# Kernel optimization log

Hardware: AMD Instinct MI355X
Metric: run time of the kernel (lower is better)

The kernel has to match this reference:

```python
import jax, jax.numpy as jnp
import numpy as np

B, T, S, L, R, H, UE = 64, 256, 16, 128, 16, 256, 64


def setup_inputs() -> dict:
    key = jax.random.key(0)
    ks = jax.random.split(key, 10)
    u = jax.random.normal(ks[0], (B, T, UE), jnp.float32)
    k = 0.1 * jax.random.normal(ks[1], (B, T, L), jnp.float32)
    K = 0.1 * jax.random.normal(ks[2], (B, T, L, R), jnp.float32)
    eps_z = jax.random.normal(ks[3], (T, S, B, L), jnp.float32)
    eps_w = jax.random.normal(ks[4], (T, S, B, R), jnp.float32)
    W1 = jax.random.normal(ks[5], (L, H), jnp.float32) / np.sqrt(L).astype(np.float32)
    W2 = jax.random.normal(ks[6], (H, L), jnp.float32) / np.sqrt(H).astype(np.float32)
    m_init = jax.random.normal(ks[7], (L,), jnp.float32)
    Q_diag = jax.random.uniform(ks[8], (L,), jnp.float32, 0.1, 1.0)
    Q0_diag = jax.random.uniform(ks[9], (L,), jnp.float32, 0.5, 1.5)
    return dict(u=u, k=k, K=K, eps_z=eps_z, eps_w=eps_w, W1=W1, W2=W2,
                m_init=m_init, Q_diag=Q_diag, Q0_diag=Q0_diag, n_samples=S)


def reference(u, k, K, eps_z, eps_w, W1, W2, m_init, Q_diag, Q0_diag, n_samples):
    Bn, Tn, Ln, Rn = K.shape
    ue = u.shape[-1]
    I_r = jnp.eye(Rn, dtype=K.dtype)

    def bmv(A, x):      # A: [B,L,R], x: [...,B,R] -> [...,B,L]
        return jnp.einsum('blr,...br->...bl', A, x)

    def bmvT(A, x):     # A: [B,L,R], x: [...,B,L] -> [...,B,R]
        return jnp.einsum('blr,...bl->...br', A, x)

    def mean_fn(z):
        return z + jnp.tanh(z @ W1) @ W2

    def step_core(m, K_t, k_t, ez, ew, q_a):
        # A = I + K^T diag(q_a) K  (rank x rank)
        A = I_r + jnp.einsum('blr,l,blq->brq', K_t, q_a, K_t)
        Lc = jnp.linalg.cholesky(A)
        Linv = jax.scipy.linalg.solve_triangular(
            Lc, jnp.broadcast_to(I_r, Lc.shape), lower=True)

        def csolve(x):  # solve A y = x via Linv^T Linv x
            y = jnp.einsum('bij,...bj->...bi', Linv, x)
            return jnp.einsum('bji,...bj->...bi', Linv, y)

        # gain direction; inner shift always uses Q_diag (as in torch source)
        g = k_t - bmv(K_t, csolve(bmvT(K_t, m + Q_diag * k_t)))
        m_f = m + q_a * g
        z_p = jnp.sqrt(q_a) * ez
        z_f = m_f + z_p - bmv(K_t, csolve(bmvT(K_t, z_p) + ew))
        qp = jnp.sum(q_a * g * g, axis=-1)
        M = A - I_r  # = K^T diag(q_a) K
        tr = -jnp.einsum('bij,bjk,bik->b', Linv, M, Linv)
        logdet = 2.0 * jnp.sum(jnp.log(jnp.diagonal(Lc, axis1=-2, axis2=-1)), axis=-1)
        kl = 0.5 * (qp + tr + logdet)
        return z_f, m_f, z_p, kl

    # ---- t = 0 (uses initial covariance Q0_diag) ----
    m0 = jnp.broadcast_to(m_init, (Bn, Ln))
    m0 = m0.at[:, :ue].add(u[:, 0])
    z_f0, m_f0, z_p0, kl0 = step_core(m0, K[:, 0], k[:, 0], eps_z[0], eps_w[0], Q0_diag)

    # ---- t = 1..T-1: sequential nonlinear filter scan ----
    def scan_fn(z_prev, xs):
        u_t, k_t, K_t, ez, ew = xs
        m = mean_fn(z_prev)            # [S,B,L]
        m = m.at[..., :ue].add(u_t)    # broadcast input over samples
        z_f, m_f, z_p, kl = step_core(m, K_t, k_t, ez, ew, Q_diag)
        return z_f, (z_f, m_f.mean(axis=0), z_p, kl.mean(axis=0))

    xs = (jnp.swapaxes(u[:, 1:], 0, 1),
          jnp.swapaxes(k[:, 1:], 0, 1),
          jnp.swapaxes(K[:, 1:], 0, 1),
          eps_z[1:], eps_w[1:])
    _, (z_fs, m_fs, z_ps, kls) = jax.lax.scan(scan_fn, z_f0, xs)

    z_f = jnp.transpose(jnp.concatenate([z_f0[None], z_fs], 0), (1, 2, 0, 3))  # [S,B,T,L]
    m_f = jnp.transpose(jnp.concatenate([m_f0[None], m_fs], 0), (1, 0, 2))     # [B,T,L]
    z_p = jnp.transpose(jnp.concatenate([z_p0[None], z_ps], 0), (1, 2, 0, 3))  # [S,B,T,L]
    kl = jnp.concatenate([kl0[None], kls], 0).T                                 # [B,T]
    return z_f, m_f, z_p, kl
```

## Files before the change

kernel.cpp:

```cpp
#include <hip/hip_runtime.h>
#include <cstddef>

typedef _Float16 half8v __attribute__((ext_vector_type(8)));
typedef _Float16 half4v __attribute__((ext_vector_type(4)));
typedef float f32x4 __attribute__((ext_vector_type(4)));

#define MFMA32(A, B, C) __builtin_amdgcn_mfma_f32_16x16x32_f16(A, B, C, 0, 0, 0)
#define MFMA16(A, B, C) __builtin_amdgcn_mfma_f32_16x16x16f16(A, B, C, 0, 0, 0)

__global__ void kw2_kernel(const float* __restrict__ W2, _Float16* __restrict__ w2h) {
  int i = blockIdx.x * 256 + threadIdx.x;
  w2h[i] = (_Float16)W2[i];
}

#define BAR() asm volatile("s_waitcnt lgkmcnt(0)\n\ts_barrier" ::: "memory")

template <bool PK, bool ZW>
__device__ __forceinline__ void scan_body(
    const int b, const int ct,
    _Float16* __restrict__ svhc, _Float16* __restrict__ hbc,
    float (*__restrict__ h2pc)[320], float (*__restrict__ qppc)[64],
    const float* __restrict__ ug, const float* __restrict__ Kg,
    const float* __restrict__ W1, const float* __restrict__ W2,
    const float* __restrict__ m_init, const float* __restrict__ Qd,
    const float* __restrict__ Q0d, const _Float16* __restrict__ pfb,
    const float* __restrict__ cgp, const _Float16* __restrict__ rfb,
    const _Float16* __restrict__ kab, const float* __restrict__ zpcb,
    const float* __restrict__ klcp, float* __restrict__ out_zf,
    float* __restrict__ out_mf, float* __restrict__ out_kl) {
  const int wvc = ct >> 6;
  const int ln = ct & 63;
  const int g = ln >> 4;
  const int c = ln & 15;

  half8v w1f[4][4];
#pragma unroll
  for (int mt = 0; mt < 4; ++mt)
#pragma unroll
    for (int kt = 0; kt < 4; ++kt) {
      half8v v;
#pragma unroll
      for (int j = 0; j < 8; ++j)
        v[j] = (_Float16)W1[(size_t)(kt * 32 + g * 8 + j) * 256 + (wvc * 64 + mt * 16 + c)];
      w1f[mt][kt] = v;
    }
  half8v w2f[2][8];
#pragma unroll
  for (int mt = 0; mt < 2; ++mt)
#pragma unroll
    for (int kt = 0; kt < 8; ++kt) {
      half8v v;
#pragma unroll
      for (int j = 0; j < 8; ++j)
        v[j] = (_Float16)W2[(size_t)(kt * 32 + g * 8 + j) * 128 + (wvc * 32 + mt * 16 + c)];
      w2f[mt][kt] = v;
    }

  f32x4 qiv[2], qiv0[2];
#pragma unroll
  for (int mt = 0; mt < 2; ++mt) {
    f32x4 q = *(const f32x4*)&Qd[wvc * 32 + mt * 16 + g * 4];
    f32x4 q0 = *(const f32x4*)&Q0d[wvc * 32 + mt * 16 + g * 4];
#pragma unroll
    for (int r = 0; r < 4; ++r) { qiv[mt][r] = 1.f / q[r]; qiv0[mt][r] = 1.f / q0[r]; }
  }

  f32x4 zreg[2];

  half8v pfx0, pfx1, kax0 = {}, kax1 = {}, rfa0, rfa1, rfc0, rfc1;
  float kf0[8], kf1[8];
  f32x4 zq0[2], zq1[2], cv0[2], cv1[2];
  f32x4 ur0[2] = {}, ur1[2] = {};
  float kv0 = 0.f, kv1 = 0.f;

  const char* pf_p = (const char*)pfb + (size_t)b * 256 * 4096 + (size_t)ct * 16;
  const char* ka_p = PK ? (const char*)kab + (size_t)b * 256 * 4096 + (size_t)ct * 16
                        : (const char*)pfb;
  const char* K_p = (const char*)Kg + (size_t)b * 256 * 8192 + (size_t)((wvc * 32 + g * 4) * 16 + c) * 4;
  const char* rf_p = (const char*)rfb + (size_t)b * 256 * 8192 + (size_t)ct * 32;
  const char* zq_p = ZW ? (const char*)zpcb + (size_t)b * 256 * 8192 + (size_t)(c * 128 + wvc * 32 + g * 4) * 4
                        : (const char*)out_zf + ((((size_t)c * 64 + b) * 256) * 128 + wvc * 32 + g * 4) * 4;
  const size_t zq_str = ZW ? 8192 : 512;
  const char* cv_p = (const char*)cgp + (size_t)b * 256 * 512 + (size_t)(wvc * 32 + g * 4) * 4;
  const char* ur_p = (const char*)ug + (size_t)b * 256 * 256 + (size_t)(wvc * 32 + g * 4) * 4;
  const char* kl_p = (const char*)klcp + (size_t)b * 256 * 4;
  char* zf_p = (char*)out_zf + ((((size_t)c * 64 + b) * 256) * 128 + wvc * 32 + g * 4) * 4;
  char* mf_p = (char*)out_mf + ((size_t)b * 256 * 128 + wvc * 32 + g * 4) * 4;

#define STAGE(BI) do { \
    pfx##BI = *(const half8v*)pf_p; pf_p += 4096; \
    if constexpr (PK) { kax##BI = *(const half8v*)ka_p; ka_p += 4096; } \
    else { _Pragma("unroll") for (int kt_ = 0; kt_ < 2; ++kt_) \
             _Pragma("unroll") for (int j_ = 0; j_ < 4; ++j_) \
               kf##BI[kt_ * 4 + j_] = *(const float*)(K_p + kt_ * 1024 + j_ * 64); \
           K_p += 8192; } \
    rfa##BI = *(const half8v*)rf_p; rfc##BI = *(const half8v*)(rf_p + 16); rf_p += 8192; \
    zq##BI[0] = *(const f32x4*)zq_p; zq##BI[1] = *(const f32x4*)(zq_p + 64); zq_p += zq_str; \
    cv##BI[0] = *(const f32x4*)cv_p; cv##BI[1] = *(const f32x4*)(cv_p + 64); cv_p += 512; \
    if (wvc < 2) { ur##BI[0] = *(const f32x4*)ur_p; ur##BI[1] = *(const f32x4*)(ur_p + 64); } \
    ur_p += 256; \
    kv##BI = *(const float*)kl_p; kl_p += 4; \
  } while (0)

#define KAH(BI, KT, DST) do { \
    if constexpr (PK) { _Pragma("unroll") for (int j_ = 0; j_ < 4; ++j_) DST[j_] = kax##BI[(KT) * 4 + j_]; } \
    else { _Pragma("unroll") for (int j_ = 0; j_ < 4; ++j_) DST[j_] = (_Float16)kf##BI[(KT) * 4 + j_]; } \
  } while (0)

#define PHASE_A(BI) do { \
    half4v zbh_[2], zbl_[2]; \
    _Pragma("unroll") for (int kt = 0; kt < 2; ++kt) \
      _Pragma("unroll") for (int j = 0; j < 4; ++j) { \
        float x_ = zreg[kt][j]; _Float16 h_ = (_Float16)x_; \
        zbh_[kt][j] = h_; zbl_[kt][j] = (_Float16)(x_ - (float)h_); } \
    half8v zh8_[4]; \
    _Pragma("unroll") for (int kt = 0; kt < 4; ++kt) { \
      int row_ = kt * 4 + g; \
      int idx_ = row_ * 128 + (((c + row_) & 15) << 3); \
      zh8_[kt] = *(const half8v*)&svhc[idx_]; } \
    f32x4 a1h_[4]; \
    _Pragma("unroll") for (int mt = 0; mt < 4; ++mt) a1h_[mt] = (f32x4){0,0,0,0}; \
    _Pragma("unroll") for (int kt = 0; kt < 4; ++kt) \
      _Pragma("unroll") for (int mt = 0; mt < 4; ++mt) \
        a1h_[mt] = MFMA32(w1f[mt][kt], zh8_[kt], a1h_[mt]); \
    half4v th_[4]; \
    _Pragma("unroll") for (int mt = 0; mt < 4; ++mt) { \
      _Pragma("unroll") for (int r = 0; r < 4; ++r) { \
        float x_ = a1h_[mt][r]; \
        float e_ = __expf(2.f * x_); \
        th_[mt][r] = (_Float16)(1.f - 2.f / (e_ + 1.f)); } \
      int row_ = wvc * 8 + mt * 2 + (g >> 1); \
      *(half4v*)&hbc[row_ * 128 + (((c + row_) & 15) << 3) + ((g & 1) << 2)] = th_[mt]; } \
    half4v ka0_, ka1_; KAH(BI, 0, ka0_); KAH(BI, 1, ka1_); \
    f32x4 hz_ = {0, 0, 0, 0}; \
    hz_ = MFMA16(ka0_, zbh_[0], hz_); hz_ = MFMA16(ka1_, zbh_[1], hz_); \
    hz_ = MFMA16(ka0_, zbl_[0], hz_); hz_ = MFMA16(ka1_, zbl_[1], hz_); \
    f32x4 hr_ = {0, 0, 0, 0}; \
    _Pragma("unroll") for (int mt = 0; mt < 4; ++mt) { \
      half4v rr_; \
      _Pragma("unroll") for (int j = 0; j < 4; ++j) \
        rr_[j] = (mt < 2) ? rfa##BI[mt * 4 + j] : rfc##BI[(mt - 2) * 4 + j]; \
      hr_ = MFMA16(rr_, th_[mt], hr_); } \
    *(f32x4*)&h2pc[wvc][c * 20 + g * 4] = hz_ + hr_; \
  } while (0)

#define EPILOG(BI, QIV, MV) do { \
    f32x4 h2v_ = *(const f32x4*)&h2pc[0][c * 20 + g * 4]; \
    h2v_ += *(const f32x4*)&h2pc[1][c * 20 + g * 4]; \
    h2v_ += *(const f32x4*)&h2pc[2][c * 20 + g * 4]; \
    h2v_ += *(const f32x4*)&h2pc[3][c * 20 + g * 4]; \
    half4v h2h_, h2l_; \
    _Pragma("unroll") for (int j = 0; j < 4; ++j) { \
      _Float16 h_ = (_Float16)h2v_[j]; \
      h2h_[j] = h_; h2l_[j] = (_Float16)(h2v_[j] - (float)h_); } \
    float qpl_ = 0.f; \
    _Pragma("unroll") for (int mt = 0; mt < 2; ++mt) { \
      half4v pfm_; \
      _Pragma("unroll") for (int j = 0; j < 4; ++j) pfm_[j] = pfx##BI[mt * 4 + j]; \
      f32x4 zz_ = {0, 0, 0, 0}; \
      f32x4 mh_ = MFMA16(pfm_, h2h_, zz_); \
      f32x4 mlv_ = MFMA16(pfm_, h2l_, zz_); \
      f32x4 dd_ = cv##BI[mt] - (mh_ + mlv_); \
      f32x4 mf_ = MV[mt] + dd_; \
      f32x4 zf_ = mf_ + zq##BI[mt]; \
      _Pragma("unroll") for (int r = 0; r < 4; ++r) qpl_ += dd_[r] * dd_[r] * QIV[mt][r]; \
      *(f32x4*)(zf_p + mt * 64) = zf_; \
      zreg[mt] = zf_; \
      half4v zh4_; \
      _Pragma("unroll") for (int r = 0; r < 4; ++r) zh4_[r] = (_Float16)zf_[r]; \
      int row_ = wvc * 4 + mt * 2 + (g >> 1); \
      int base_ = row_ * 128 + (((c + row_) & 15) << 3) + ((g & 1) << 2); \
      *(half4v*)&svhc[base_] = zh4_; \
      f32x4 ms_ = mf_; \
      _Pragma("unroll") for (int r = 0; r < 4; ++r) { \
        float x_ = ms_[r]; \
        x_ += __shfl_xor(x_, 1); x_ += __shfl_xor(x_, 2); \
        x_ += __shfl_xor(x_, 4); x_ += __shfl_xor(x_, 8); \
        ms_[r] = x_ * 0.0625f; } \
      if (c == 0) *(f32x4*)(mf_p + mt * 64) = ms_; \
    } \
    zf_p += 512; mf_p += 512; \
    qpl_ += __shfl_xor(qpl_, 16); \
    qpl_ += __shfl_xor(qpl_, 32); \
    if (g == 0) qppc[BI][wvc * 16 + c] = qpl_; \
  } while (0)

#define PHASE_B(BI, QIV) do { \
    half8v hf_[8]; \
    _Pragma("unroll") for (int kt = 0; kt < 8; ++kt) { \
      int row_ = kt * 4 + g; \
      hf_[kt] = *(const half8v*)&hbc[row_ * 128 + (((c + row_) & 15) << 3)]; } \
    f32x4 a2a_[2], a2b_[2]; \
    _Pragma("unroll") for (int mt = 0; mt < 2; ++mt) { a2a_[mt] = (f32x4){0,0,0,0}; a2b_[mt] = (f32x4){0,0,0,0}; } \
    _Pragma("unroll") for (int kt = 0; kt < 4; ++kt) \
      _Pragma("unroll") for (int mt = 0; mt < 2; ++mt) { \
        a2a_[mt] = MFMA32(w2f[mt][kt], hf_[kt], a2a_[mt]); \
        a2b_[mt] = MFMA32(w2f[mt][kt + 4], hf_[kt + 4], a2b_[mt]); } \
    f32x4 mv_[2]; \
    _Pragma("unroll") for (int mt = 0; mt < 2; ++mt) { \
      mv_[mt] = zreg[mt] + a2a_[mt] + a2b_[mt]; \
      if (wvc < 2) mv_[mt] += ur##BI[mt]; } \
    EPILOG(BI, QIV, mv_); \
  } while (0)

#define KL_FIN(PBI, TPREV) do { \
    if (ct < 16) { \
      float v_ = qppc[PBI][ct] + qppc[PBI][16 + ct] + qppc[PBI][32 + ct] + qppc[PBI][48 + ct]; \
      v_ += __shfl_xor(v_, 1); v_ += __shfl_xor(v_, 2); \
      v_ += __shfl_xor(v_, 4); v_ += __shfl_xor(v_, 8); \
      if (ct == 0) out_kl[(size_t)b * 256 + (size_t)(TPREV)] = 0.03125f * v_ + kv##PBI; \
    } \
  } while (0)

  STAGE(0);
  STAGE(1);
  {
    f32x4 mv0[2];
#pragma unroll
    for (int mt = 0; mt < 2; ++mt) {
      mv0[mt] = *(const f32x4*)&m_init[wvc * 32 + mt * 16 + g * 4];
      if (wvc < 2) mv0[mt] += ur0[mt];
    }
    half4v mh0[2], ml0[2];
#pragma unroll
    for (int kt = 0; kt < 2; ++kt)
#pragma unroll
      for (int j = 0; j < 4; ++j) {
        float x = mv0[kt][j];
        _Float16 h = (_Float16)x;
        mh0[kt][j] = h;
        ml0[kt][j] = (_Float16)(x - (float)h);
      }
    half4v ka0_, ka1_;
    KAH(0, 0, ka0_); KAH(0, 1, ka1_);
    f32x4 hz = {0, 0, 0, 0};
    hz = MFMA16(ka0_, mh0[0], hz); hz = MFMA16(ka1_, mh0[1], hz);
    hz = MFMA16(ka0_, ml0[0], hz); hz = MFMA16(ka1_, ml0[1], hz);
    *(f32x4*)&h2pc[wvc][c * 20 + g * 4] = hz;
    BAR();
    EPILOG(0, qiv0, mv0);
    BAR();
  }

  for (int t = 1; t < 255; t += 2) {
    KL_FIN(0, t - 1);
    STAGE(0);
    PHASE_A(1);
    BAR();
    PHASE_B(1, qiv);
    BAR();
    KL_FIN(1, t);
    STAGE(1);
    PHASE_A(0);
    BAR();
    PHASE_B(0, qiv);
    BAR();
  }
  KL_FIN(0, 254);
  PHASE_A(1);
  BAR();
  PHASE_B(1, qiv);
  BAR();
  KL_FIN(1, 255);

#undef STAGE
#undef KAH
#undef PHASE_A
#undef EPILOG
#undef PHASE_B
#undef KL_FIN
}

template <bool PK, bool ZW>
__launch_bounds__(256, 1)
__global__ void kscan1_kernel(const float* __restrict__ ug, const float* __restrict__ Kg,
                              const float* __restrict__ W1, const float* __restrict__ W2,
                              const float* __restrict__ m_init, const float* __restrict__ Qd,
                              const float* __restrict__ Q0d, const _Float16* __restrict__ pfb,
                              const float* __restrict__ cgp, const _Float16* __restrict__ rfb,
                              const _Float16* __restrict__ kab, const float* __restrict__ zpcb,
                              const float* __restrict__ klcp, float* __restrict__ out_zf,
                              float* __restrict__ out_mf, float* __restrict__ out_kl) {
  __shared__ __align__(16) _Float16 svh[2048];
  __shared__ __align__(16) _Float16 hb[4096];
  __shared__ float h2p[4][320];
  __shared__ float qpp[2][64];
  scan_body<PK, ZW>(blockIdx.x, threadIdx.x, svh, hb, h2p, qpp,
                    ug, Kg, W1, W2, m_init, Qd, Q0d, pfb, cgp, rfb, kab, zpcb, klcp,
                    out_zf, out_mf, out_kl);
}

__global__ void kprep1_kernel(const float* __restrict__ Kg, const float* __restrict__ kg,
                              const float* __restrict__ ug, const float* __restrict__ Qd,
                              const float* __restrict__ Q0d, float* __restrict__ Ainv,
                              float* __restrict__ klc, _Float16* __restrict__ pfb,
                              float* __restrict__ cgp, _Float16* __restrict__ kab) {
  int tid = threadIdx.x;
  int wv = tid >> 6, ln = tid & 63;
  size_t bt = (size_t)blockIdx.x * 4 + wv;
  int t = (int)(bt & 255);
  __shared__ __align__(16) float Ks[4][128][20];
  __shared__ float qs[4][128];
  __shared__ float vvs[4][128];
  __shared__ float Asm[4][16][20];
  __shared__ float LiL[4][16][20];
  __shared__ float AiS[4][16][20];
  __shared__ float yps[4][4][16];
  __shared__ float yvs[4][16];
  const f32x4* kp4 = (const f32x4*)(Kg + bt * 2048);
  for (int i = ln; i < 512; i += 64) {
    f32x4 v = kp4[i];
    *(f32x4*)&Ks[wv][i >> 2][(i & 3) * 4] = v;
  }
  for (int l = ln; l < 128; l += 64) {
    float q = (t == 0) ? Q0d[l] : Qd[l];
    qs[wv][l] = q;
    float v = Qd[l] * kg[bt * 128 + l];
    if (t > 0 && l < 64) v += ug[bt * 64 + l];
    vvs[wv][l] = v;
  }
  __syncthreads();
  if (kab) {
    int gg = ln >> 4, cc2 = ln & 15;
#pragma unroll
    for (int q = 0; q < 4; ++q) {
      half8v ko;
#pragma unroll
      for (int kt = 0; kt < 2; ++kt)
#pragma unroll
        for (int j = 0; j < 4; ++j)
          ko[kt * 4 + j] = (_Float16)Ks[wv][q * 32 + kt * 16 + gg * 4 + j][cc2];
      *(half8v*)(kab + bt * 2048 + (size_t)(q * 64 + ln) * 8) = ko;
    }
  }
  {
    int r = ln & 15, c0 = (ln >> 4) << 2;
    float a0 = 0, a1 = 0, a2 = 0, a3 = 0;
    for (int l = 0; l < 128; ++l) {
      float kq = Ks[wv][l][r] * qs[wv][l];
      const float* row = &Ks[wv][l][c0];
      a0 += kq * row[0]; a1 += kq * row[1]; a2 += kq * row[2]; a3 += kq * row[3];
    }
    Asm[wv][r][c0 + 0] = a0 + ((r == c0 + 0) ? 1.f : 0.f);
    Asm[wv][r][c0 + 1] = a1 + ((r == c0 + 1) ? 1.f : 0.f);
    Asm[wv][r][c0 + 2] = a2 + ((r == c0 + 2) ? 1.f : 0.f);
    Asm[wv][r][c0 + 3] = a3 + ((r == c0 + 3) ? 1.f : 0.f);
  }
  {
    int r = ln & 15, seg = ln >> 4;
    float s = 0.f;
    for (int l = seg * 32; l < seg * 32 + 32; ++l) s += Ks[wv][l][r] * vvs[wv][l];
    yps[wv][seg][r] = s;
  }
  __syncthreads();
  if (ln < 16) {
    int i = ln;
    float ar[16], Lr[16];
#pragma unroll
    for (int j = 0; j < 16; ++j) ar[j] = Asm[wv][i][j];
    float ld = 0.f;
#pragma unroll
    for (int j = 0; j < 16; ++j) {
      float ajj = __shfl(ar[j], j, 64);
      float d = sqrtf(ajj);
      ld += __logf(d);
      float li = ar[j] / d;
      li = (i >= j) ? li : 0.f;
      Lr[j] = li;
#pragma unroll
      for (int k2 = j; k2 < 16; ++k2) {
        float lk = __shfl(li, k2, 64);
        ar[k2] -= li * lk;
      }
    }
    int cc = i;
    float Lic[16];
#pragma unroll
    for (int ii = 0; ii < 16; ++ii) {
      float s = (ii == cc) ? 1.f : 0.f;
#pragma unroll
      for (int p = 0; p < 16; ++p) {
        if (p < ii) {
          float Lip = __shfl(Lr[p], ii, 64);
          s -= Lip * Lic[p];
        }
      }
      float dii = __shfl(Lr[ii], ii, 64);
      float v = s / dii;
      Lic[ii] = (ii >= cc) ? v : 0.f;
    }
    float tr = 0.f;
#pragma unroll
    for (int ii = 0; ii < 16; ++ii) { tr += Lic[ii] * Lic[ii]; LiL[wv][cc][ii] = Lic[ii]; }
    tr += __shfl_xor(tr, 1); tr += __shfl_xor(tr, 2);
    tr += __shfl_xor(tr, 4); tr += __shfl_xor(tr, 8);
    if (cc == 0) klc[bt] = 0.5f * (tr - 16.f + 2.f * ld);
    yvs[wv][cc] = yps[wv][0][cc] + yps[wv][1][cc] + yps[wv][2][cc] + yps[wv][3][cc];
  }
  __syncthreads();
  {
    int r = ln & 15, c0 = (ln >> 4) << 2;
    float a0 = 0, a1 = 0, a2 = 0, a3 = 0;
    for (int ii = 0; ii < 16; ++ii) {
      float lir = LiL[wv][r][ii];
      a0 += lir * LiL[wv][c0 + 0][ii];
      a1 += lir * LiL[wv][c0 + 1][ii];
      a2 += lir * LiL[wv][c0 + 2][ii];
      a3 += lir * LiL[wv][c0 + 3][ii];
    }
    AiS[wv][r][c0 + 0] = a0; AiS[wv][r][c0 + 1] = a1;
    AiS[wv][r][c0 + 2] = a2; AiS[wv][r][c0 + 3] = a3;
    f32x4 av = {a0, a1, a2, a3};
    *(f32x4*)&Ainv[bt * 256 + r * 16 + c0] = av;
  }
  __syncthreads();
  {
#pragma unroll
    for (int li = 0; li < 2; ++li) {
      int l = ln * 2 + li;
      f32x4 acc0 = {0,0,0,0}, acc1v = {0,0,0,0}, acc2v = {0,0,0,0}, acc3v = {0,0,0,0};
      for (int j = 0; j < 16; ++j) {
        float kj = Ks[wv][l][j];
        acc0  += kj * *(const f32x4*)&AiS[wv][j][0];
        acc1v += kj * *(const f32x4*)&AiS[wv][j][4];
        acc2v += kj * *(const f32x4*)&AiS[wv][j][8];
        acc3v += kj * *(const f32x4*)&AiS[wv][j][12];
      }
      float ql = qs[wv][l];
      float cp = ql * kg[bt * 128 + l];
      float pv[16];
#pragma unroll
      for (int e = 0; e < 4; ++e) {
        pv[e] = ql * acc0[e]; pv[4 + e] = ql * acc1v[e];
        pv[8 + e] = ql * acc2v[e]; pv[12 + e] = ql * acc3v[e];
      }
#pragma unroll
      for (int r = 0; r < 16; ++r) cp -= pv[r] * yvs[wv][r];
      cgp[bt * 128 + l] = cp;
#pragma unroll
      for (int r = 0; r < 16; ++r) Ks[wv][l][r] = pv[r];
    }
  }
  __syncthreads();
  {
    int gp = ln >> 4, cp = ln & 15;
#pragma unroll
    for (int ci = 0; ci < 4; ++ci) {
      half8v o;
#pragma unroll
      for (int mt = 0; mt < 2; ++mt)
#pragma unroll
        for (int j = 0; j < 4; ++j)
          o[mt * 4 + j] = (_Float16)Ks[wv][ci * 32 + mt * 16 + cp][gp * 4 + j];
      *(half8v*)(pfb + bt * 2048 + (size_t)(ci * 64 + ln) * 8) = o;
    }
  }
}

__global__ void kc3_kernel(const _Float16* __restrict__ kab, const float* __restrict__ epsz,
                           const float* __restrict__ epsw, const float* __restrict__ Qd,
                           const float* __restrict__ Q0d, const float* __restrict__ Ainv,
                           const _Float16* __restrict__ w2h,
                           _Float16* __restrict__ rfb,
                           float* __restrict__ zpcb, float* __restrict__ out_zp) {
  int idx = blockIdx.x;
  int t = idx >> 6, b = idx & 63;
  size_t bt = (size_t)b * 256 + t;
  int tid = threadIdx.x;
  const int wv = tid >> 6, ln = tid & 63, g = ln >> 4, c = ln & 15;
  __shared__ _Float16 Ksh[128][18];
  __shared__ float Ai[16][16];
  __shared__ __align__(16) float zp[16][132];
  __shared__ float hh[16][17];
  __shared__ float ww[16][17];
  __shared__ float sq[128];
  __shared__ _Float16 Rh[16][264];
  {
    half8v ko = *(const half8v*)(kab + bt * 2048 + (size_t)tid * 8);
#pragma unroll
    for (int kt = 0; kt < 2; ++kt)
#pragma unroll
      for (int j = 0; j < 4; ++j)
        Ksh[wv * 32 + kt * 16 + g * 4 + j][c] = ko[kt * 4 + j];
  }
  ((float*)Ai)[tid] = Ainv[bt * 256 + tid];
  const float* q = (t == 0) ? Q0d : Qd;
  if (tid < 128) sq[tid] = sqrtf(q[tid]);
  __syncthreads();
  {
    const f32x4* ez4 = (const f32x4*)(epsz + ((size_t)t * 16 * 64) * 128);
    f32x4* ozp4 = (f32x4*)out_zp;
    for (int i = tid; i < 512; i += 256) {
      int s = i >> 5, l4 = i & 31;
      f32x4 e = ez4[((size_t)s * 64 + b) * 32 + l4];
      f32x4 sv = *(const f32x4*)&sq[l4 * 4];
      f32x4 v = e * sv;
      *(f32x4*)&zp[s][l4 * 4] = v;
      ozp4[(((size_t)s * 64 + b) * 256 + t) * 32 + l4] = v;
    }
  }
  {
    half8v kA[4];
#pragma unroll
    for (int kt = 0; kt < 4; ++kt)
#pragma unroll
      for (int j = 0; j < 8; ++j) kA[kt][j] = Ksh[kt * 32 + g * 8 + j][c];
#pragma unroll
    for (int i = 0; i < 4; ++i) {
      int tile = wv * 4 + i;
      f32x4 acc = {0, 0, 0, 0};
#pragma unroll
      for (int kt = 0; kt < 4; ++kt) {
        half8v bf = *(const half8v*)&w2h[(size_t)(tile * 16 + c) * 128 + kt * 32 + g * 8];
        acc = MFMA32(kA[kt], bf, acc);
      }
#pragma unroll
      for (int r = 0; r < 4; ++r) Rh[g * 4 + r][tile * 16 + c] = (_Float16)acc[r];
    }
  }
  __syncthreads();
  {
    int s = tid >> 4, r = tid & 15;
    float acc = epsw[(((size_t)t * 16 + s) * 64 + b) * 16 + r];
    for (int l = 0; l < 128; ++l) acc += (float)Ksh[l][r] * zp[s][l];
    hh[s][r] = acc;
  }
  {
    half8v r0, r1;
#pragma unroll
    for (int mt = 0; mt < 4; ++mt)
#pragma unroll
      for (int j = 0; j < 4; ++j) {
        _Float16 v = Rh[c][wv * 64 + mt * 16 + g * 4 + j];
        if (mt < 2) r0[mt * 4 + j] = v; else r1[(mt - 2) * 4 + j] = v;
      }
    *(half8v*)(rfb + bt * 4096 + (size_t)tid * 16) = r0;
    *(half8v*)(rfb + bt * 4096 + (size_t)tid * 16 + 8) = r1;
  }
  __syncthreads();
  {
    int s = tid >> 4, r = tid & 15;
    float acc = 0.f;
    for (int j = 0; j < 16; ++j) acc += Ai[r][j] * hh[s][j];
    ww[s][r] = acc;
  }
  __syncthreads();
  for (int i = tid; i < 2048; i += 256) {
    int s = i >> 7, l = i & 127;
    float acc = 0.f;
    for (int r = 0; r < 16; ++r) acc += (float)Ksh[l][r] * ww[s][r];
    zpcb[bt * 2048 + i] = zp[s][l] - acc;
  }
}

__global__ void kprepR_kernel(const float* __restrict__ Kg, const _Float16* __restrict__ w2h,
                              _Float16* __restrict__ rfb, _Float16* __restrict__ kab) {
  int tid = threadIdx.x;
  int wv = tid >> 6, ln = tid & 63;
  int g = ln >> 4, c = ln & 15;
  __shared__ _Float16 Kh[128][20];
  __shared__ _Float16 Rh[16][264];
  for (int it = 0; it < 4; ++it) {
    size_t bt = (size_t)blockIdx.x * 4 + it;
    const float* kp = Kg + bt * 2048;
    for (int i = tid; i < 2048; i += 256) Kh[i >> 4][i & 15] = (_Float16)kp[i];
    __syncthreads();
    half8v kA[4];
#pragma unroll
    for (int kt = 0; kt < 4; ++kt)
#pragma unroll
      for (int j = 0; j < 8; ++j) kA[kt][j] = Kh[kt * 32 + g * 8 + j][c];
#pragma unroll
    for (int i = 0; i < 4; ++i) {
      int tile = wv * 4 + i;
      f32x4 acc = {0, 0, 0, 0};
#pragma unroll
      for (int kt = 0; kt < 4; ++kt) {
        half8v bf = *(const half8v*)&w2h[(size_t)(tile * 16 + c) * 128 + kt * 32 + g * 8];
        acc = MFMA32(kA[kt], bf, acc);
      }
#pragma unroll
      for (int r = 0; r < 4; ++r) Rh[g * 4 + r][tile * 16 + c] = (_Float16)acc[r];
    }
    __syncthreads();
    half8v r0, r1;
#pragma unroll
    for (int mt = 0; mt < 4; ++mt)
#pragma unroll
      for (int j = 0; j < 4; ++j) {
        _Float16 v = Rh[c][wv * 64 + mt * 16 + g * 4 + j];
        if (mt < 2) r0[mt * 4 + j] = v; else r1[(mt - 2) * 4 + j] = v;
      }
    *(half8v*)(rfb + bt * 4096 + (size_t)tid * 16) = r0;
    *(half8v*)(rfb + bt * 4096 + (size_t)tid * 16 + 8) = r1;
    if (kab) {
      half8v ko;
#pragma unroll
      for (int kt = 0; kt < 2; ++kt)
#pragma unroll
        for (int j = 0; j < 4; ++j) ko[kt * 4 + j] = Kh[wv * 32 + kt * 16 + g * 4 + j][c];
      *(half8v*)(kab + bt * 2048 + (size_t)tid * 8) = ko;
    }
    __syncthreads();
  }
}

__global__ void kc_kernel(const float* __restrict__ Kg, const float* __restrict__ epsz,
                          const float* __restrict__ epsw, const float* __restrict__ Qd,
                          const float* __restrict__ Q0d, const float* __restrict__ Ainv,
                          float* __restrict__ out_zf, float* __restrict__ out_zp,
                          float* __restrict__ zpcb, int zw, int wzp) {
  int idx = blockIdx.x;
  int t = idx >> 6, b = idx & 63;
  int bt = b * 256 + t;
  __shared__ float Ks[128][16];
  __shared__ float Ai[16][16];
  __shared__ float zp[16][129];
  __shared__ float hh[16][17];
  __shared__ float ww[16][17];
  __shared__ float sq[128];
  const float* kp = Kg + (size_t)bt * 2048;
  for (int i = threadIdx.x; i < 2048; i += 256) ((float*)Ks)[i] = kp[i];
  ((float*)Ai)[threadIdx.x] = Ainv[(size_t)bt * 256 + threadIdx.x];
  const float* q = (t == 0) ? Q0d : Qd;
  if (threadIdx.x < 128) sq[threadIdx.x] = sqrtf(q[threadIdx.x]);
  __syncthreads();
  for (int i = threadIdx.x; i < 2048; i += 256) {
    int s = i >> 7, l = i & 127;
    float v = sq[l] * epsz[(((size_t)t * 16 + s) * 64 + b) * 128 + l];
    zp[s][l] = v;
    if (wzp) out_zp[(((size_t)s * 64 + b) * 256 + t) * 128 + l] = v;
  }
  __syncthreads();
  {
    int s = threadIdx.x >> 4, r = threadIdx.x & 15;
    float acc = epsw[(((size_t)t * 16 + s) * 64 + b) * 16 + r];
    for (int l = 0; l < 128; ++l) acc += Ks[l][r] * zp[s][l];
    hh[s][r] = acc;
  }
  __syncthreads();
  {
    int s = threadIdx.x >> 4, r = threadIdx.x & 15;
    float acc = 0.f;
    for (int j = 0; j < 16; ++j) acc += Ai[r][j] * hh[s][j];
    ww[s][r] = acc;
  }
  __syncthreads();
  for (int i = threadIdx.x; i < 2048; i += 256) {
    int s = i >> 7, l = i & 127;
    float acc = 0.f;
    for (int r = 0; r < 16; ++r) acc += Ks[l][r] * ww[s][r];
    float v = zp[s][l] - acc;
    if (zw) zpcb[(size_t)bt * 2048 + i] = v;
    else out_zf[(((size_t)s * 64 + b) * 256 + t) * 128 + l] = v;
  }
}

__global__ void kzp_kernel(const float* __restrict__ epsz, const float* __restrict__ Qd,
                           const float* __restrict__ Q0d, float* __restrict__ out_zp) {
  for (size_t i = (size_t)blockIdx.x * blockDim.x + threadIdx.x; i < (size_t)33554432;
       i += (size_t)gridDim.x * blockDim.x) {
    int l = (int)(i & 127);
    int t = (int)((i >> 7) & 255);
    int sb = (int)(i >> 15);
    int s = sb >> 6, b = sb & 63;
    float q = (t == 0) ? Q0d[l] : Qd[l];
    out_zp[i] = sqrtf(q) * epsz[(((size_t)t * 16 + s) * 64 + b) * 128 + l];
  }
}

extern "C" void kernel_launch(void* const* d_in, const int* in_sizes, int n_in,
                              void* d_out, int out_size, void* d_ws, size_t ws_size,
                              hipStream_t stream) {
  (void)in_sizes; (void)n_in; (void)out_size;
  const float* u   = (const float*)d_in[0];
  const float* kk  = (const float*)d_in[1];
  const float* Kg  = (const float*)d_in[2];
  const float* epz = (const float*)d_in[3];
  const float* epw = (const float*)d_in[4];
  const float* W1  = (const float*)d_in[5];
  const float* W2  = (const float*)d_in[6];
  const float* mi  = (const float*)d_in[7];
  const float* Qd  = (const float*)d_in[8];
  const float* Q0d = (const float*)d_in[9];

  float* out_zf = (float*)d_out;
  float* out_mf = out_zf + (size_t)33554432;
  float* out_zp = out_mf + (size_t)2097152;
  float* out_kl = out_zp + (size_t)33554432;

  char* ws = (char*)d_ws;

  const size_t F_klc  = 0;
  const size_t F_cgp  = 65536;
  const size_t F_pfb  = 8454144;
  const size_t F_w2h  = 75563008;
  const size_t F_kab  = 75628544;
  const size_t F_rfb  = 142737408;
  const size_t F_zpc  = 276955136;
  const size_t F_ainv = 411172864;
  const size_t F_END  = 427950080;

  if (ws_size >= F_END) {
    float*    klc  = (float*)(ws + F_klc);
    float*    cgp  = (float*)(ws + F_cgp);
    _Float16* pfb  = (_Float16*)(ws + F_pfb);
    _Float16* w2h  = (_Float16*)(ws + F_w2h);
    _Float16* kab  = (_Float16*)(ws + F_kab);
    _Float16* rfb  = (_Float16*)(ws + F_rfb);
    float*    zpcb = (float*)(ws + F_zpc);
    float*    Ainv = (float*)(ws + F_ainv);
    kw2_kernel<<<128, 256, 0, stream>>>(W2, w2h);
    kprep1_kernel<<<4096, 256, 0, stream>>>(Kg, kk, u, Qd, Q0d, Ainv, klc, pfb, cgp, kab);
    kc3_kernel<<<16384, 256, 0, stream>>>(kab, epz, epw, Qd, Q0d, Ainv, w2h,
                                          rfb, zpcb, out_zp);
    kscan1_kernel<true, true><<<64, 256, 0, stream>>>(u, Kg, W1, W2, mi, Qd, Q0d, pfb,
                                                      cgp, rfb, kab, zpcb, klc,
                                                      out_zf, out_mf, out_kl);
    return;
  }

  size_t off = 0;
  auto take = [&](size_t n) { char* p = ws + off; off += n; return p; };
  float*    Ainv = (float*)take(16777216);
  float*    klc  = (float*)take(65536);
  float*    cgp  = (float*)take(8388608);
  _Float16* pfb  = (_Float16*)take(67108864);
  _Float16* w2h  = (_Float16*)take(65536);
  bool zw = ws_size >= off + 134217728;
  float* zpcb = zw ? (float*)take(134217728) : nullptr;
  bool pk = zw && (ws_size >= off + 67108864);
  _Float16* kab = pk ? (_Float16*)take(67108864) : nullptr;
  bool rfws = ws_size >= off + 134217728;
  _Float16* rfb = rfws ? (_Float16*)take(134217728) : (_Float16*)out_zp;
  int wzp = rfws ? 1 : 0;

  kw2_kernel<<<128, 256, 0, stream>>>(W2, w2h);
  kprep1_kernel<<<4096, 256, 0, stream>>>(Kg, kk, u, Qd, Q0d, Ainv, klc, pfb, cgp, nullptr);
  kprepR_kernel<<<4096, 256, 0, stream>>>(Kg, w2h, rfb, kab);
  kc_kernel<<<16384, 256, 0, stream>>>(Kg, epz, epw, Qd, Q0d, Ainv, out_zf, out_zp,
                                       zpcb, zw ? 1 : 0, wzp);
  if (pk)
    kscan1_kernel<true, true><<<64, 256, 0, stream>>>(u, Kg, W1, W2, mi, Qd, Q0d, pfb, cgp, rfb, kab, zpcb, klc, out_zf, out_mf, out_kl);
  else if (zw)
    kscan1_kernel<false, true><<<64, 256, 0, stream>>>(u, Kg, W1, W2, mi, Qd, Q0d, pfb, cgp, rfb, kab, zpcb, klc, out_zf, out_mf, out_kl);
  else
    kscan1_kernel<false, false><<<64, 256, 0, stream>>>(u, Kg, W1, W2, mi, Qd, Q0d, pfb, cgp, rfb, kab, zpcb, klc, out_zf, out_mf, out_kl);
  if (!rfws) kzp_kernel<<<2048, 256, 0, stream>>>(epz, Qd, Q0d, out_zp);
}
```

Measured before the change: 1.007 ms.

## Fuse per-timestep precompute into scan kernel with flag-based producer-consumer sync

Merges the kc3 precompute kernel and the sequential scan kernel into one launch. The first 64 blocks run the scan and the remaining blocks compute per-(b,t) inputs. Each producer block publishes a release flag when it finishes, and scan blocks spin with an acquire load on the flag for timestep t before staging it. This lets the long serial scan overlap with the bulk precompute instead of waiting for the whole kc3 grid to finish. The cost is a flag memset, spin-waiting, and a dependence on the scan blocks being scheduled first so the spins cannot deadlock.

```diff
diff --git a/kernel.cpp b/kernel.cpp
--- a/kernel.cpp
+++ b/kernel.cpp
@@ -27,11 +27,17 @@
     const float* __restrict__ cgp, const _Float16* __restrict__ rfb,
     const _Float16* __restrict__ kab, const float* __restrict__ zpcb,
     const float* __restrict__ klcp, float* __restrict__ out_zf,
-    float* __restrict__ out_mf, float* __restrict__ out_kl) {
+    float* __restrict__ out_mf, float* __restrict__ out_kl,
+    unsigned* flags) {
   const int wvc = ct >> 6;
   const int ln = ct & 63;
   const int g = ln >> 4;
   const int c = ln & 15;
+
+#define WAITF(T) do { if (flags) { \
+    unsigned* fp_ = flags + ((size_t)b * 256 + (size_t)(T)); \
+    while (__hip_atomic_load(fp_, __ATOMIC_ACQUIRE, __HIP_MEMORY_SCOPE_AGENT) == 0u) \
+      __builtin_amdgcn_s_sleep(8); } } while (0)
 
   half8v w1f[4][4];
 #pragma unroll
@@ -212,7 +218,9 @@
     } \
   } while (0)
 
+  WAITF(0);
   STAGE(0);
+  WAITF(1);
   STAGE(1);
   {
     f32x4 mv0[2];
@@ -244,12 +252,14 @@
 
   for (int t = 1; t < 255; t += 2) {
     KL_FIN(0, t - 1);
+    WAITF(t + 1);
     STAGE(0);
     PHASE_A(1);
     BAR();
     PHASE_B(1, qiv);
     BAR();
     KL_FIN(1, t);
+    WAITF(t + 2);
     STAGE(1);
     PHASE_A(0);
     BAR();
@@ -269,6 +279,102 @@
 #undef EPILOG
 #undef PHASE_B
 #undef KL_FIN
+#undef WAITF
+}
+
+__device__ __forceinline__ void kc3_body(
+    const int idx, const int tid, char* __restrict__ raw,
+    const _Float16* __restrict__ kab, const float* __restrict__ epsz,
+    const float* __restrict__ epsw, const float* __restrict__ Qd,
+    const float* __restrict__ Q0d, const float* __restrict__ Ainv,
+    const _Float16* __restrict__ w2h, _Float16* __restrict__ rfb,
+    float* __restrict__ zpcb, float* __restrict__ out_zp) {
+  int t = idx >> 6, b = idx & 63;
+  size_t bt = (size_t)b * 256 + t;
+  const int wv = tid >> 6, ln = tid & 63, g = ln >> 4, c = ln & 15;
+  _Float16 (*Ksh)[18] = (_Float16 (*)[18])raw;
+  float* sq = (float*)(raw + 4608);
+  float (*Ai)[16] = (float (*)[16])(raw + 5120);
+  float (*hh)[17] = (float (*)[17])(raw + 6144);
+  float (*ww)[17] = (float (*)[17])(raw + 7232);
+  float (*zp)[132] = (float (*)[132])(raw + 8320);
+  _Float16 (*Rh)[264] = (_Float16 (*)[264])(raw + 16768);
+  {
+    half8v ko = *(const half8v*)(kab + bt * 2048 + (size_t)tid * 8);
+#pragma unroll
+    for (int kt = 0; kt < 2; ++kt)
+#pragma unroll
+      for (int j = 0; j < 4; ++j)
+        Ksh[wv * 32 + kt * 16 + g * 4 + j][c] = ko[kt * 4 + j];
+  }
+  ((float*)Ai)[tid] = Ainv[bt * 256 + tid];
+  const float* q = (t == 0) ? Q0d : Qd;
+  if (tid < 128) sq[tid] = sqrtf(q[tid]);
+  __syncthreads();
+  {
+    const f32x4* ez4 = (const f32x4*)(epsz + ((size_t)t * 16 * 64) * 128);
+    f32x4* ozp4 = (f32x4*)out_zp;
+    for (int i = tid; i < 512; i += 256) {
+      int s = i >> 5, l4 = i & 31;
+      f32x4 e = ez4[((size_t)s * 64 + b) * 32 + l4];
+      f32x4 sv = *(const f32x4*)&sq[l4 * 4];
+      f32x4 v = e * sv;
+      *(f32x4*)&zp[s][l4 * 4] = v;
+      ozp4[(((size_t)s * 64 + b) * 256 + t) * 32 + l4] = v;
+    }
+  }
+  {
+    half8v kA[4];
+#pragma unroll
+    for (int kt = 0; kt < 4; ++kt)
+#pragma unroll
+      for (int j = 0; j < 8; ++j) kA[kt][j] = Ksh[kt * 32 + g * 8 + j][c];
+#pragma unroll
+    for (int i = 0; i < 4; ++i) {
+      int tile = wv * 4 + i;
+      f32x4 acc = {0, 0, 0, 0};
+#pragma unroll
+      for (int kt = 0; kt < 4; ++kt) {
+        half8v bf = *(const half8v*)&w2h[(size_t)(tile * 16 + c) * 128 + kt * 32 + g * 8];
+        acc = MFMA32(kA[kt], bf, acc);
+      }
+#pragma unroll
+      for (int r = 0; r < 4; ++r) Rh[g * 4 + r][tile * 16 + c] = (_Float16)acc[r];
+    }
+  }
+  __syncthreads();
+  {
+    int s = tid >> 4, r = tid & 15;
+    float acc = epsw[(((size_t)t * 16 + s) * 64 + b) * 16 + r];
+    for (int l = 0; l < 128; ++l) acc += (float)Ksh[l][r] * zp[s][l];
+    hh[s][r] = acc;
+  }
+  {
+    half8v r0, r1;
+#pragma unroll
+    for (int mt = 0; mt < 4; ++mt)
+#pragma unroll
+      for (int j = 0; j < 4; ++j) {
+        _Float16 v = Rh[c][wv * 64 + mt * 16 + g * 4 + j];
+        if (mt < 2) r0[mt * 4 + j] = v; else r1[(mt - 2) * 4 + j] = v;
+      }
+    *(half8v*)(rfb + bt * 4096 + (size_t)tid * 16) = r0;
+    *(half8v*)(rfb + bt * 4096 + (size_t)tid * 16 + 8) = r1;
+  }
+  __syncthreads();
+  {
+    int s = tid >> 4, r = tid & 15;
+    float acc = 0.f;
+    for (int j = 0; j < 16; ++j) acc += Ai[r][j] * hh[s][j];
+    ww[s][r] = acc;
+  }
+  __syncthreads();
+  for (int i = tid; i < 2048; i += 256) {
+    int s = i >> 7, l = i & 127;
+    float acc = 0.f;
+    for (int r = 0; r < 16; ++r) acc += (float)Ksh[l][r] * ww[s][r];
+    zpcb[bt * 2048 + i] = zp[s][l] - acc;
+  }
 }
 
 template <bool PK, bool ZW>
@@ -287,7 +393,52 @@
   __shared__ float qpp[2][64];
   scan_body<PK, ZW>(blockIdx.x, threadIdx.x, svh, hb, h2p, qpp,
                     ug, Kg, W1, W2, m_init, Qd, Q0d, pfb, cgp, rfb, kab, zpcb, klcp,
-                    out_zf, out_mf, out_kl);
+                    out_zf, out_mf, out_kl, nullptr);
+}
+
+__global__ void kc3_kernel(const _Float16* __restrict__ kab, const float* __restrict__ epsz,
+                           const float* __restrict__ epsw, const float* __restrict__ Qd,
+                           const float* __restrict__ Q0d, const float* __restrict__ Ainv,
+                           const _Float16* __restrict__ w2h, _Float16* __restrict__ rfb,
+                           float* __restrict__ zpcb, float* __restrict__ out_zp) {
+  __shared__ __align__(16) char raw[25216];
+  kc3_body(blockIdx.x, threadIdx.x, raw, kab, epsz, epsw, Qd, Q0d, Ainv, w2h, rfb, zpcb, out_zp);
+}
+
+__launch_bounds__(256, 1)
+__global__ void fused2_kernel(const float* __restrict__ ug, const float* __restrict__ Kg,
+                              const float* __restrict__ W1, const float* __restrict__ W2,
+                              const float* __restrict__ m_init, const float* __restrict__ Qd,
+                              const float* __restrict__ Q0d, const _Float16* __restrict__ pfb,
+                              const float* __restrict__ cgp, _Float16* __restrict__ rfb,
+                              const _Float16* __restrict__ kab, float* __restrict__ zpcb,
+                              const float* __restrict__ klcp,
+                              const float* __restrict__ epsz, const float* __restrict__ epsw,
+                              const float* __restrict__ Ainv, const _Float16* __restrict__ w2h,
+                              unsigned* __restrict__ flags,
+                              float* __restrict__ out_zf, float* __restrict__ out_mf,
+                              float* __restrict__ out_zp, float* __restrict__ out_kl) {
+  __shared__ __align__(16) char raw[25216];
+  const int tid = threadIdx.x;
+  if (blockIdx.x < 64) {
+    _Float16* svh = (_Float16*)raw;
+    _Float16* hb = (_Float16*)(raw + 4096);
+    float (*h2p)[320] = (float (*)[320])(raw + 12288);
+    float (*qpp)[64] = (float (*)[64])(raw + 17408);
+    scan_body<true, true>(blockIdx.x, tid, svh, hb, h2p, qpp,
+                          ug, Kg, W1, W2, m_init, Qd, Q0d, pfb, cgp, rfb, kab,
+                          zpcb, klcp, out_zf, out_mf, out_kl, flags);
+    return;
+  }
+  const int idx = (int)blockIdx.x - 64;
+  kc3_body(idx, tid, raw, kab, epsz, epsw, Qd, Q0d, Ainv, w2h, rfb, zpcb, out_zp);
+  __syncthreads();
+  if (tid == 0) {
+    int t = idx >> 6, b = idx & 63;
+    __threadfence();
+    __hip_atomic_store(&flags[(size_t)b * 256 + t], 1u, __ATOMIC_RELEASE,
+                       __HIP_MEMORY_SCOPE_AGENT);
+  }
 }
 
 __global__ void kprep1_kernel(const float* __restrict__ Kg, const float* __restrict__ kg,
@@ -457,102 +608,6 @@
   }
 }
 
-__global__ void kc3_kernel(const _Float16* __restrict__ kab, const float* __restrict__ epsz,
-                           const float* __restrict__ epsw, const float* __restrict__ Qd,
-                           const float* __restrict__ Q0d, const float* __restrict__ Ainv,
-                           const _Float16* __restrict__ w2h,
-                           _Float16* __restrict__ rfb,
-                           float* __restrict__ zpcb, float* __restrict__ out_zp) {
-  int idx = blockIdx.x;
-  int t = idx >> 6, b = idx & 63;
-  size_t bt = (size_t)b * 256 + t;
-  int tid = threadIdx.x;
-  const int wv = tid >> 6, ln = tid & 63, g = ln >> 4, c = ln & 15;
-  __shared__ _Float16 Ksh[128][18];
-  __shared__ float Ai[16][16];
-  __shared__ __align__(16) float zp[16][132];
-  __shared__ float hh[16][17];
-  __shared__ float ww[16][17];
-  __shared__ float sq[128];
-  __shared__ _Float16 Rh[16][264];
-  {
-    half8v ko = *(const half8v*)(kab + bt * 2048 + (size_t)tid * 8);
-#pragma unroll
-    for (int kt = 0; kt < 2; ++kt)
-#pragma unroll
-      for (int j = 0; j < 4; ++j)
-        Ksh[wv * 32 + kt * 16 + g * 4 + j][c] = ko[kt * 4 + j];
-  }
-  ((float*)Ai)[tid] = Ainv[bt * 256 + tid];
-  const float* q = (t == 0) ? Q0d : Qd;
-  if (tid < 128) sq[tid] = sqrtf(q[tid]);
-  __syncthreads();
-  {
-    const f32x4* ez4 = (const f32x4*)(epsz + ((size_t)t * 16 * 64) * 128);
-    f32x4* ozp4 = (f32x4*)out_zp;
-    for (int i = tid; i < 512; i += 256) {
-      int s = i >> 5, l4 = i & 31;
-      f32x4 e = ez4[((size_t)s * 64 + b) * 32 + l4];
-      f32x4 sv = *(const f32x4*)&sq[l4 * 4];
-      f32x4 v = e * sv;
-      *(f32x4*)&zp[s][l4 * 4] = v;
-      ozp4[(((size_t)s * 64 + b) * 256 + t) * 32 + l4] = v;
-    }
-  }
-  {
-    half8v kA[4];
-#pragma unroll
-    for (int kt = 0; kt < 4; ++kt)
-#pragma unroll
-      for (int j = 0; j < 8; ++j) kA[kt][j] = Ksh[kt * 32 + g * 8 + j][c];
-#pragma unroll
-    for (int i = 0; i < 4; ++i) {
-      int tile = wv * 4 + i;
-      f32x4 acc = {0, 0, 0, 0};
-#pragma unroll
-      for (int kt = 0; kt < 4; ++kt) {
-        half8v bf = *(const half8v*)&w2h[(size_t)(tile * 16 + c) * 128 + kt * 32 + g * 8];
-        acc = MFMA32(kA[kt], bf, acc);
-      }
-#pragma unroll
-      for (int r = 0; r < 4; ++r) Rh[g * 4 + r][tile * 16 + c] = (_Float16)acc[r];
-    }
-  }
-  __syncthreads();
-  {
-    int s = tid >> 4, r = tid & 15;
-    float acc = epsw[(((size_t)t * 16 + s) * 64 + b) * 16 + r];
-    for (int l = 0; l < 128; ++l) acc += (float)Ksh[l][r] * zp[s][l];
-    hh[s][r] = acc;
-  }
-  {
-    half8v r0, r1;
-#pragma unroll
-    for (int mt = 0; mt < 4; ++mt)
-#pragma unroll
-      for (int j = 0; j < 4; ++j) {
-        _Float16 v = Rh[c][wv * 64 + mt * 16 + g * 4 + j];
-        if (mt < 2) r0[mt * 4 + j] = v; else r1[(mt - 2) * 4 + j] = v;
-      }
-    *(half8v*)(rfb + bt * 4096 + (size_t)tid * 16) = r0;
-    *(half8v*)(rfb + bt * 4096 + (size_t)tid * 16 + 8) = r1;
-  }
-  __syncthreads();
-  {
-    int s = tid >> 4, r = tid & 15;
-    float acc = 0.f;
-    for (int j = 0; j < 16; ++j) acc += Ai[r][j] * hh[s][j];
-    ww[s][r] = acc;
-  }
-  __syncthreads();
-  for (int i = tid; i < 2048; i += 256) {
-    int s = i >> 7, l = i & 127;
-    float acc = 0.f;
-    for (int r = 0; r < 16; ++r) acc += (float)Ksh[l][r] * ww[s][r];
-    zpcb[bt * 2048 + i] = zp[s][l] - acc;
-  }
-}
-
 __global__ void kprepR_kernel(const float* __restrict__ Kg, const _Float16* __restrict__ w2h,
                               _Float16* __restrict__ rfb, _Float16* __restrict__ kab) {
   int tid = threadIdx.x;
@@ -699,9 +754,11 @@
   const size_t F_rfb  = 142737408;
   const size_t F_zpc  = 276955136;
   const size_t F_ainv = 411172864;
-  const size_t F_END  = 427950080;
-
-  if (ws_size >= F_END) {
+  const size_t F_MID  = 427950080;
+  const size_t F_flg  = 427950080;
+  const size_t F_END  = 428015616;
+
+  if (ws_size >= F_MID) {
     float*    klc  = (float*)(ws + F_klc);
     float*    cgp  = (float*)(ws + F_cgp);
     _Float16* pfb  = (_Float16*)(ws + F_pfb);
@@ -710,13 +767,30 @@
     _Float16* rfb  = (_Float16*)(ws + F_rfb);
     float*    zpcb = (float*)(ws + F_zpc);
     float*    Ainv = (float*)(ws + F_ainv);
+
+    bool fuse = ws_size >= F_END;
+    if (fuse) {
+      hipFuncAttributes fa;
+      if (hipFuncGetAttributes(&fa, (const void*)fused2_kernel) != hipSuccess ||
+          fa.localSizeBytes != 0)
+        fuse = false;
+    }
+
     kw2_kernel<<<128, 256, 0, stream>>>(W2, w2h);
     kprep1_kernel<<<4096, 256, 0, stream>>>(Kg, kk, u, Qd, Q0d, Ainv, klc, pfb, cgp, kab);
-    kc3_kernel<<<16384, 256, 0, stream>>>(kab, epz, epw, Qd, Q0d, Ainv, w2h,
-                                          rfb, zpcb, out_zp);
-    kscan1_kernel<true, true><<<64, 256, 0, stream>>>(u, Kg, W1, W2, mi, Qd, Q0d, pfb,
-                                                      cgp, rfb, kab, zpcb, klc,
-                                                      out_zf, out_mf, out_kl);
+    if (fuse) {
+      unsigned* flags = (unsigned*)(ws + F_flg);
+      (void)hipMemsetAsync(flags, 0, 65536, stream);
+      fused2_kernel<<<16448, 256, 0, stream>>>(u, Kg, W1, W2, mi, Qd, Q0d, pfb, cgp,
+                                               rfb, kab, zpcb, klc, epz, epw, Ainv, w2h,
+                                               flags, out_zf, out_mf, out_zp, out_kl);
+    } else {
+      kc3_kernel<<<16384, 256, 0, stream>>>(kab, epz, epw, Qd, Q0d, Ainv, w2h,
+                                            rfb, zpcb, out_zp);
+      kscan1_kernel<true, true><<<64, 256, 0, stream>>>(u, Kg, W1, W2, mi, Qd, Q0d, pfb,
+                                                        cgp, rfb, kab, zpcb, klc,
+                                                        out_zf, out_mf, out_kl);
+    }
     return;
   }
 
```

After: 2.128 ms. 2.11x slower.
